# Kernel tuning notes

Hardware: AMD Instinct MI355X
Metric: run time of the kernel (lower is better)

## Reference

```python
import jax, jax.numpy as jnp
import numpy as np

N = 50000      # nodes
E = 800000     # edges
R = 8          # relation types
IN = 128       # in_dim
OUT = 128      # out_dim
H = 8          # num_heads
HD = OUT // H  # head dim = 16


def setup_inputs() -> dict:
    key = jax.random.key(0)
    ks = jax.random.split(key, 6)
    return {
        "h": jax.random.normal(ks[0], (N, IN), dtype=jnp.float32),
        "fc_weight": jax.random.normal(ks[1], (R, IN, OUT), dtype=jnp.float32) * 0.05,
        "attn_weight": jax.random.normal(ks[2], (R, H, 2 * HD), dtype=jnp.float32) * 0.05,
        "src": jax.random.randint(ks[3], (E,), 0, N, dtype=jnp.int32),
        "dst": jax.random.randint(ks[4], (E,), 0, N, dtype=jnp.int32),
        "etype": jax.random.randint(ks[5], (E,), 0, R, dtype=jnp.int32),
    }


def reference(h, fc_weight, attn_weight, src, dst, etype):
    # Per-relation projection of ALL node features (equivalent math to the
    # per-edge gathered bmm in the original, without materializing E x IN x OUT):
    # [R, N, OUT] -> [R, N, H, HD]
    z_nodes = jnp.einsum('ni,rio->rno', h, fc_weight).reshape(R, N, H, HD)
    z_s = z_nodes[etype, src]   # [E, H, HD]  (== bmm(h[src], fc_weight[etype]))
    z_d = z_nodes[etype, dst]   # [E, H, HD]
    aw = attn_weight[etype]     # [E, H, 2*HD]
    # a = sum(cat([z_s, z_d], -1) * attn_weight[etype], -1)
    a = jnp.sum(z_s * aw[:, :, :HD], axis=2) + jnp.sum(z_d * aw[:, :, HD:], axis=2)  # [E, H]
    e = jax.nn.leaky_relu(a)    # torch F.leaky_relu_ default slope 0.01

    # Edge softmax per destination node (per head), numerically stable.
    m = jax.ops.segment_max(e, dst, num_segments=N)          # [N, H]
    m = jnp.where(jnp.isfinite(m), m, jnp.zeros_like(m))     # guard empty nodes
    ex = jnp.exp(e - m[dst])                                 # [E, H]
    denom = jax.ops.segment_sum(ex, dst, num_segments=N)     # [N, H]
    num = jax.ops.segment_sum(ex[:, :, None] * z_s, dst, num_segments=N)  # [N, H, HD]
    out = num / jnp.maximum(denom, 1e-9)[:, :, None]         # [N, H, HD]
    return out
```

## Files before the change

kernel.cpp:

```cpp
#include <hip/hip_runtime.h>

#define NN 50000
#define NE 800000
#define NR 8
#define DIN 128
#define DOUT 128
#define NH 8

#define NB_SCAN ((NN + 255) / 256)

typedef __attribute__((ext_vector_type(8))) short bf16x8;
typedef __attribute__((ext_vector_type(4))) float f32x4;

__device__ __forceinline__ unsigned short f2bf(float f) {
  unsigned u = __float_as_uint(f);
  unsigned r = (u + 0x7FFFu + ((u >> 16) & 1u)) >> 16;
  return (unsigned short)r;
}
__device__ __forceinline__ float bf2f(unsigned short b) {
  return __uint_as_float(((unsigned)b) << 16);
}

__global__ __launch_bounds__(256) void prep_fcf(
    const float* __restrict__ fc, const float* __restrict__ attn,
    unsigned short* __restrict__ fcf) {
  int idx = blockIdx.x * 256 + threadIdx.x;
  if (idx >= NR * DIN * 144) return;
  int r = idx / (DIN * 144);
  int rem = idx - r * (DIN * 144);
  int k = rem / 144;
  int j = rem - k * 144;
  float v;
  if (j < DOUT) {
    v = fc[((size_t)r * DIN + k) * DOUT + j];
  } else {
    int cc = j - DOUT;
    int hh = cc & 7, p = cc >> 3;
    const float* fr = fc + ((size_t)r * DIN + k) * DOUT + hh * 16;
    const float* ar = attn + ((size_t)r * NH + hh) * 32 + p * 16;
    v = 0.f;
#pragma unroll
    for (int d = 0; d < 16; ++d) v += fr[d] * ar[d];
  }
  int t = j >> 4, c = j & 15, ks = k >> 5, gg = (k >> 3) & 3, i = k & 7;
  fcf[((((size_t)r * 9 + t) * 4 + ks) * 4 + gg) * 128 + c * 8 + i] = f2bf(v);
}

__global__ __launch_bounds__(256) void gemm_mfma(
    const float* __restrict__ h, const unsigned short* __restrict__ fcf,
    unsigned short* __restrict__ z, unsigned short* __restrict__ s_buf) {
  const int n0 = blockIdx.x * 64;
  const int rr0 = blockIdx.y * 4;
  const int w = threadIdx.x >> 6;
  const int lane = threadIdx.x & 63;
  const int g = lane >> 4, c = lane & 15;
  const int nbase = n0 + w * 16;

  __shared__ unsigned short zst[4][16][130];

  int arow = nbase + c;
  if (arow > NN - 1) arow = NN - 1;
  const float* ha = h + (size_t)arow * DIN + g * 8;
  bf16x8 af[4];
#pragma unroll
  for (int ks = 0; ks < 4; ++ks) {
    float4 v0 = *(const float4*)(ha + ks * 32);
    float4 v1 = *(const float4*)(ha + ks * 32 + 4);
    bf16x8 a;
    a[0] = (short)f2bf(v0.x); a[1] = (short)f2bf(v0.y);
    a[2] = (short)f2bf(v0.z); a[3] = (short)f2bf(v0.w);
    a[4] = (short)f2bf(v1.x); a[5] = (short)f2bf(v1.y);
    a[6] = (short)f2bf(v1.z); a[7] = (short)f2bf(v1.w);
    af[ks] = a;
  }

  const int node = nbase + c;

  for (int ri = 0; ri < 4; ++ri) {
    const int r = rr0 + ri;
    const unsigned short* fb = fcf + ((size_t)r * 36 * 64 + lane) * 8;
    f32x4 acc[9];
#pragma unroll
    for (int t = 0; t < 9; ++t) acc[t] = (f32x4){0.f, 0.f, 0.f, 0.f};

#pragma unroll
    for (int ks = 0; ks < 4; ++ks)
#pragma unroll
      for (int t = 0; t < 9; ++t) {
        bf16x8 bf = *(const bf16x8*)(fb + (size_t)(t * 4 + ks) * 512);
        acc[t] = __builtin_amdgcn_mfma_f32_16x16x32_bf16(bf, af[ks], acc[t], 0, 0, 0);
      }

#pragma unroll
    for (int t = 0; t < 8; ++t) {
      ushort4 wv;
      wv.x = f2bf(acc[t][0]); wv.y = f2bf(acc[t][1]);
      wv.z = f2bf(acc[t][2]); wv.w = f2bf(acc[t][3]);
      *(ushort4*)&zst[w][c][t * 16 + g * 4] = wv;
    }
    __builtin_amdgcn_s_waitcnt(0);
    unsigned short* zb = z + ((size_t)r * NN + nbase) * DOUT;
#pragma unroll
    for (int p = 0; p < 4; ++p) {
      int row = 4 * p + (lane >> 4);
      if (nbase + row < NN) {
        bf16x8 v = *(const bf16x8*)&zst[w][row][(lane & 15) * 8];
        *(bf16x8*)(zb + row * DOUT + (lane & 15) * 8) = v;
      }
    }

    if (node < NN) {
      ushort4 sv;
      sv.x = f2bf(acc[8][0]); sv.y = f2bf(acc[8][1]);
      sv.z = f2bf(acc[8][2]); sv.w = f2bf(acc[8][3]);
      *(ushort4*)&s_buf[((size_t)r * NN + node) * 16 + g * 4] = sv;
    }
  }
}

__global__ __launch_bounds__(256) void hist_kernel(const int* __restrict__ dst,
                                                   int* __restrict__ deg) {
  int e = blockIdx.x * blockDim.x + threadIdx.x;
  if (e < NE) atomicAdd(&deg[dst[e]], 1);
}

__global__ __launch_bounds__(256) void scan1(const int* __restrict__ deg,
                                             int* __restrict__ bsum) {
  __shared__ int ws_[4];
  int gi = blockIdx.x * 256 + threadIdx.x;
  int v = (gi < NN) ? deg[gi] : 0;
#pragma unroll
  for (int m = 1; m < 64; m <<= 1) v += __shfl_xor(v, m);
  if ((threadIdx.x & 63) == 0) ws_[threadIdx.x >> 6] = v;
  __syncthreads();
  if (threadIdx.x == 0) bsum[blockIdx.x] = ws_[0] + ws_[1] + ws_[2] + ws_[3];
}

__global__ __launch_bounds__(256) void scan2(const int* __restrict__ bsum,
                                             int* __restrict__ bbase,
                                             int* __restrict__ row_start) {
  __shared__ int part[256];
  int t = threadIdx.x;
  part[t] = (t < NB_SCAN) ? bsum[t] : 0;
  __syncthreads();
  for (int off = 1; off < 256; off <<= 1) {
    int v = (t >= off) ? part[t - off] : 0;
    __syncthreads();
    part[t] += v;
    __syncthreads();
  }
  if (t < NB_SCAN) bbase[t] = (t == 0) ? 0 : part[t - 1];
  if (t == 0) row_start[NN] = NE;
}

__global__ __launch_bounds__(256) void scan3(const int* __restrict__ deg,
                                             const int* __restrict__ bbase,
                                             int* __restrict__ row_start) {
  __shared__ int part[256];
  int t = threadIdx.x;
  int gi = blockIdx.x * 256 + t;
  int v = (gi < NN) ? deg[gi] : 0;
  part[t] = v;
  __syncthreads();
  for (int off = 1; off < 256; off <<= 1) {
    int x = (t >= off) ? part[t - off] : 0;
    __syncthreads();
    part[t] += x;
    __syncthreads();
  }
  if (gi < NN) row_start[gi] = bbase[blockIdx.x] + part[t] - v;
}

__global__ __launch_bounds__(256) void scatter_kernel(
    const int* __restrict__ src, const int* __restrict__ dst,
    const int* __restrict__ et, const int* __restrict__ row_start,
    int* __restrict__ cursor, unsigned* __restrict__ sidx) {
  int e = blockIdx.x * blockDim.x + threadIdx.x;
  if (e >= NE) return;
  int d = dst[e];
  int pos = row_start[d] + atomicAdd(&cursor[d], 1);
  sidx[pos] = (unsigned)src[e] | ((unsigned)et[e] << 16);
}

__global__ __launch_bounds__(256) void node_accum(
    const int* __restrict__ row_start, const unsigned* __restrict__ sidx,
    const unsigned short* __restrict__ s_buf, const unsigned short* __restrict__ z,
    float* __restrict__ out) {
  int wave = threadIdx.x >> 6;
  int lane = threadIdx.x & 63;
  int n = blockIdx.x * 4 + wave;
  if (n >= NN) return;
  int b0 = row_start[n];
  int deg = row_start[n + 1] - b0;

  int hl = lane & 7;
  int jg = lane >> 3;
  int c16 = lane & 15;
  int e4 = lane >> 4;
  int hh16 = c16 >> 1;

  float srn[8];
#pragma unroll
  for (int r = 0; r < 8; ++r)
    srn[r] = bf2f(s_buf[((size_t)r * NN + n) * 16 + 8 + hl]);

  float m = -INFINITY;
  float den = 0.f;
  float acc[8] = {0.f, 0.f, 0.f, 0.f, 0.f, 0.f, 0.f, 0.f};

  for (int cch = 0; cch < deg; cch += 8) {
    int j = cch + jg;
    int rem = min(8, deg - cch);
    float ev = -INFINITY;
    unsigned pj = 0;
    if (j < deg) {
      pj = sidx[b0 + j];
      unsigned s = pj & 0xFFFFu, r = pj >> 16;
      float sl = bf2f(s_buf[((size_t)r * NN + s) * 16 + hl]);
      float x = sl + srn[r];
      ev = x > 0.f ? x : 0.01f * x;
    }
    float cm = ev;
    cm = fmaxf(cm, __shfl_xor(cm, 8));
    cm = fmaxf(cm, __shfl_xor(cm, 16));
    cm = fmaxf(cm, __shfl_xor(cm, 32));
    float newm = fmaxf(m, cm);
    float scale = __expf(m - newm);
    float ex = __expf(ev - newm);
    float sumex = ex;
    sumex += __shfl_xor(sumex, 8);
    sumex += __shfl_xor(sumex, 16);
    sumex += __shfl_xor(sumex, 32);
    den = den * scale + sumex;
    m = newm;
    float sc_acc = __shfl(scale, hh16);
#pragma unroll
    for (int i = 0; i < 8; ++i) acc[i] *= sc_acc;
#pragma unroll
    for (int half = 0; half < 2; ++half) {
      if (half * 4 >= rem) break;
      int o = half * 4 + e4;
      float exb = __shfl(ex, (o << 3) | hh16);
      unsigned p = __shfl(pj, o << 3);
      unsigned sr_ = p & 0xFFFFu;
      unsigned rr = p >> 16;
      bf16x8 v = *(const bf16x8*)&z[(((size_t)rr * NN + sr_) << 7) + c16 * 8];
#pragma unroll
      for (int i = 0; i < 8; ++i)
        acc[i] += exb * bf2f((unsigned short)v[i]);
    }
  }
#pragma unroll
  for (int i = 0; i < 8; ++i) {
    acc[i] += __shfl_xor(acc[i], 16);
    acc[i] += __shfl_xor(acc[i], 32);
  }
  float deno = __shfl(den, hh16);
  float inv = 1.0f / fmaxf(deno, 1e-9f);
  if (lane < 16) {
    float* ob = out + ((size_t)n << 7) + lane * 8;
    *(float4*)ob = make_float4(acc[0] * inv, acc[1] * inv, acc[2] * inv, acc[3] * inv);
    *(float4*)(ob + 4) = make_float4(acc[4] * inv, acc[5] * inv, acc[6] * inv, acc[7] * inv);
  }
}

extern "C" void kernel_launch(void* const* d_in, const int* in_sizes, int n_in,
                              void* d_out, int out_size, void* d_ws, size_t ws_size,
                              hipStream_t stream) {
  const float* h = (const float*)d_in[0];
  const float* fc = (const float*)d_in[1];
  const float* attn = (const float*)d_in[2];
  const int* src = (const int*)d_in[3];
  const int* dst = (const int*)d_in[4];
  const int* et = (const int*)d_in[5];
  float* out = (float*)d_out;

  char* wsb = (char*)d_ws;
  size_t off = 0;
  unsigned short* z = (unsigned short*)(wsb + off);    off += (size_t)NR * NN * DOUT * 2;
  unsigned short* s_buf = (unsigned short*)(wsb + off);off += (size_t)NR * NN * 16 * 2;
  unsigned* sidx = (unsigned*)(wsb + off);             off += (size_t)NE * 4;
  unsigned short* fcf = (unsigned short*)(wsb + off);  off += (size_t)NR * 9 * 4 * 4 * 128 * 2;
  int* deg = (int*)(wsb + off);                        off += (size_t)NN * 4;
  int* row_start = (int*)(wsb + off);                  off += (size_t)(NN + 1) * 4;
  int* cursor = (int*)(wsb + off);                     off += (size_t)NN * 4;
  int* bsum = (int*)(wsb + off);                       off += (size_t)NB_SCAN * 4;
  int* bbase = (int*)(wsb + off);                      off += (size_t)NB_SCAN * 4;

  hipMemsetAsync(deg, 0, (size_t)NN * sizeof(int), stream);
  hipMemsetAsync(cursor, 0, (size_t)NN * sizeof(int), stream);

  prep_fcf<<<(NR * DIN * 144 + 255) / 256, 256, 0, stream>>>(fc, attn, fcf);

  dim3 ggrid((NN + 63) / 64, 2);
  gemm_mfma<<<ggrid, 256, 0, stream>>>(h, fcf, z, s_buf);

  hist_kernel<<<(NE + 255) / 256, 256, 0, stream>>>(dst, deg);
  scan1<<<NB_SCAN, 256, 0, stream>>>(deg, bsum);
  scan2<<<1, 256, 0, stream>>>(bsum, bbase, row_start);
  scan3<<<NB_SCAN, 256, 0, stream>>>(deg, bbase, row_start);

  scatter_kernel<<<(NE + 255) / 256, 256, 0, stream>>>(src, dst, et, row_start,
                                                       cursor, sidx);

  node_accum<<<(NN + 3) / 4, 256, 0, stream>>>(row_start, sidx, s_buf, z, out);
}
```

Baseline: 274.5 us.

## Fuse weight prep and CSR construction into one cooperative kernel with grid syncs

Replaces two memsets and six separate launches (weight folding, histogram, three scan stages, scatter) with a single cooperative kernel. The kernel runs 196 blocks and separates the phases with grid.sync(). This removes per-launch overhead and gaps between the small kernels. In exchange, the atomic histogram and scatter run on far fewer threads via grid-stride loops, and each grid barrier has its own cost.

```diff
diff --git a/kernel.cpp b/kernel.cpp
--- a/kernel.cpp
+++ b/kernel.cpp
@@ -1,4 +1,7 @@
 #include <hip/hip_runtime.h>
+#include <hip/hip_cooperative_groups.h>
+
+namespace cg = cooperative_groups;
 
 #define NN 50000
 #define NE 800000
@@ -21,29 +24,96 @@
   return __uint_as_float(((unsigned)b) << 16);
 }
 
-__global__ __launch_bounds__(256) void prep_fcf(
+__global__ __launch_bounds__(256) void build_csr(
     const float* __restrict__ fc, const float* __restrict__ attn,
-    unsigned short* __restrict__ fcf) {
-  int idx = blockIdx.x * 256 + threadIdx.x;
-  if (idx >= NR * DIN * 144) return;
-  int r = idx / (DIN * 144);
-  int rem = idx - r * (DIN * 144);
-  int k = rem / 144;
-  int j = rem - k * 144;
-  float v;
-  if (j < DOUT) {
-    v = fc[((size_t)r * DIN + k) * DOUT + j];
-  } else {
-    int cc = j - DOUT;
-    int hh = cc & 7, p = cc >> 3;
-    const float* fr = fc + ((size_t)r * DIN + k) * DOUT + hh * 16;
-    const float* ar = attn + ((size_t)r * NH + hh) * 32 + p * 16;
-    v = 0.f;
-#pragma unroll
-    for (int d = 0; d < 16; ++d) v += fr[d] * ar[d];
-  }
-  int t = j >> 4, c = j & 15, ks = k >> 5, gg = (k >> 3) & 3, i = k & 7;
-  fcf[((((size_t)r * 9 + t) * 4 + ks) * 4 + gg) * 128 + c * 8 + i] = f2bf(v);
+    unsigned short* __restrict__ fcf, const int* __restrict__ src,
+    const int* __restrict__ dst, const int* __restrict__ et,
+    int* __restrict__ deg, int* __restrict__ cursor,
+    int* __restrict__ row_start, int* __restrict__ bsum,
+    int* __restrict__ bbase, unsigned* __restrict__ sidx) {
+  cg::grid_group grid = cg::this_grid();
+  const int tid = blockIdx.x * 256 + threadIdx.x;
+  const int nth = gridDim.x * 256;
+
+  for (int i = tid; i < NN; i += nth) {
+    deg[i] = 0;
+    cursor[i] = 0;
+  }
+  for (int idx = tid; idx < NR * DIN * 144; idx += nth) {
+    int r = idx / (DIN * 144);
+    int rem2 = idx - r * (DIN * 144);
+    int k = rem2 / 144;
+    int j = rem2 - k * 144;
+    float v;
+    if (j < DOUT) {
+      v = fc[((size_t)r * DIN + k) * DOUT + j];
+    } else {
+      int cc = j - DOUT;
+      int hh = cc & 7, p = cc >> 3;
+      const float* fr = fc + ((size_t)r * DIN + k) * DOUT + hh * 16;
+      const float* ar = attn + ((size_t)r * NH + hh) * 32 + p * 16;
+      v = 0.f;
+#pragma unroll
+      for (int d = 0; d < 16; ++d) v += fr[d] * ar[d];
+    }
+    int t = j >> 4, c = j & 15, ks = k >> 5, gg = (k >> 3) & 3, i = k & 7;
+    fcf[((((size_t)r * 9 + t) * 4 + ks) * 4 + gg) * 128 + c * 8 + i] = f2bf(v);
+  }
+  grid.sync();
+
+  for (int e = tid; e < NE; e += nth) atomicAdd(&deg[dst[e]], 1);
+  grid.sync();
+
+  {
+    __shared__ int ws_[4];
+    int gi = blockIdx.x * 256 + threadIdx.x;
+    int v = (gi < NN) ? deg[gi] : 0;
+#pragma unroll
+    for (int m = 1; m < 64; m <<= 1) v += __shfl_xor(v, m);
+    if ((threadIdx.x & 63) == 0) ws_[threadIdx.x >> 6] = v;
+    __syncthreads();
+    if (threadIdx.x == 0) bsum[blockIdx.x] = ws_[0] + ws_[1] + ws_[2] + ws_[3];
+  }
+  grid.sync();
+
+  if (blockIdx.x == 0) {
+    __shared__ int part[256];
+    int t = threadIdx.x;
+    part[t] = (t < NB_SCAN) ? bsum[t] : 0;
+    __syncthreads();
+    for (int off = 1; off < 256; off <<= 1) {
+      int v = (t >= off) ? part[t - off] : 0;
+      __syncthreads();
+      part[t] += v;
+      __syncthreads();
+    }
+    if (t < NB_SCAN) bbase[t] = (t == 0) ? 0 : part[t - 1];
+    if (t == 0) row_start[NN] = NE;
+  }
+  grid.sync();
+
+  {
+    __shared__ int part[256];
+    int t = threadIdx.x;
+    int gi = blockIdx.x * 256 + t;
+    int v = (gi < NN) ? deg[gi] : 0;
+    part[t] = v;
+    __syncthreads();
+    for (int off = 1; off < 256; off <<= 1) {
+      int x = (t >= off) ? part[t - off] : 0;
+      __syncthreads();
+      part[t] += x;
+      __syncthreads();
+    }
+    if (gi < NN) row_start[gi] = bbase[blockIdx.x] + part[t] - v;
+  }
+  grid.sync();
+
+  for (int e = tid; e < NE; e += nth) {
+    int d = dst[e];
+    int pos = row_start[d] + atomicAdd(&cursor[d], 1);
+    sidx[pos] = (unsigned)src[e] | ((unsigned)et[e] << 16);
+  }
 }
 
 __global__ __launch_bounds__(256) void gemm_mfma(
@@ -116,70 +186,6 @@
       *(ushort4*)&s_buf[((size_t)r * NN + node) * 16 + g * 4] = sv;
     }
   }
-}
-
-__global__ __launch_bounds__(256) void hist_kernel(const int* __restrict__ dst,
-                                                   int* __restrict__ deg) {
-  int e = blockIdx.x * blockDim.x + threadIdx.x;
-  if (e < NE) atomicAdd(&deg[dst[e]], 1);
-}
-
-__global__ __launch_bounds__(256) void scan1(const int* __restrict__ deg,
-                                             int* __restrict__ bsum) {
-  __shared__ int ws_[4];
-  int gi = blockIdx.x * 256 + threadIdx.x;
-  int v = (gi < NN) ? deg[gi] : 0;
-#pragma unroll
-  for (int m = 1; m < 64; m <<= 1) v += __shfl_xor(v, m);
-  if ((threadIdx.x & 63) == 0) ws_[threadIdx.x >> 6] = v;
-  __syncthreads();
-  if (threadIdx.x == 0) bsum[blockIdx.x] = ws_[0] + ws_[1] + ws_[2] + ws_[3];
-}
-
-__global__ __launch_bounds__(256) void scan2(const int* __restrict__ bsum,
-                                             int* __restrict__ bbase,
-                                             int* __restrict__ row_start) {
-  __shared__ int part[256];
-  int t = threadIdx.x;
-  part[t] = (t < NB_SCAN) ? bsum[t] : 0;
-  __syncthreads();
-  for (int off = 1; off < 256; off <<= 1) {
-    int v = (t >= off) ? part[t - off] : 0;
-    __syncthreads();
-    part[t] += v;
-    __syncthreads();
-  }
-  if (t < NB_SCAN) bbase[t] = (t == 0) ? 0 : part[t - 1];
-  if (t == 0) row_start[NN] = NE;
-}
-
-__global__ __launch_bounds__(256) void scan3(const int* __restrict__ deg,
-                                             const int* __restrict__ bbase,
-                                             int* __restrict__ row_start) {
-  __shared__ int part[256];
-  int t = threadIdx.x;
-  int gi = blockIdx.x * 256 + t;
-  int v = (gi < NN) ? deg[gi] : 0;
-  part[t] = v;
-  __syncthreads();
-  for (int off = 1; off < 256; off <<= 1) {
-    int x = (t >= off) ? part[t - off] : 0;
-    __syncthreads();
-    part[t] += x;
-    __syncthreads();
-  }
-  if (gi < NN) row_start[gi] = bbase[blockIdx.x] + part[t] - v;
-}
-
-__global__ __launch_bounds__(256) void scatter_kernel(
-    const int* __restrict__ src, const int* __restrict__ dst,
-    const int* __restrict__ et, const int* __restrict__ row_start,
-    int* __restrict__ cursor, unsigned* __restrict__ sidx) {
-  int e = blockIdx.x * blockDim.x + threadIdx.x;
-  if (e >= NE) return;
-  int d = dst[e];
-  int pos = row_start[d] + atomicAdd(&cursor[d], 1);
-  sidx[pos] = (unsigned)src[e] | ((unsigned)et[e] << 16);
 }
 
 __global__ __launch_bounds__(256) void node_accum(
@@ -287,21 +293,14 @@
   int* bsum = (int*)(wsb + off);                       off += (size_t)NB_SCAN * 4;
   int* bbase = (int*)(wsb + off);                      off += (size_t)NB_SCAN * 4;
 
-  hipMemsetAsync(deg, 0, (size_t)NN * sizeof(int), stream);
-  hipMemsetAsync(cursor, 0, (size_t)NN * sizeof(int), stream);
-
-  prep_fcf<<<(NR * DIN * 144 + 255) / 256, 256, 0, stream>>>(fc, attn, fcf);
+  void* args[] = {(void*)&fc,  (void*)&attn,   (void*)&fcf,    (void*)&src,
+                  (void*)&dst, (void*)&et,     (void*)&deg,    (void*)&cursor,
+                  (void*)&row_start, (void*)&bsum, (void*)&bbase, (void*)&sidx};
+  hipLaunchCooperativeKernel((void*)build_csr, dim3(NB_SCAN), dim3(256), args, 0,
+                             stream);
 
   dim3 ggrid((NN + 63) / 64, 2);
   gemm_mfma<<<ggrid, 256, 0, stream>>>(h, fcf, z, s_buf);
 
-  hist_kernel<<<(NE + 255) / 256, 256, 0, stream>>>(dst, deg);
-  scan1<<<NB_SCAN, 256, 0, stream>>>(deg, bsum);
-  scan2<<<1, 256, 0, stream>>>(bsum, bbase, row_start);
-  scan3<<<NB_SCAN, 256, 0, stream>>>(deg, bbase, row_start);
-
-  scatter_kernel<<<(NE + 255) / 256, 256, 0, stream>>>(src, dst, et, row_start,
-                                                       cursor, sidx);
-
   node_accum<<<(NN + 3) / 4, 256, 0, stream>>>(row_start, sidx, s_buf, z, out);
 }
```

After: 377.4 us. +37.5%, slower.
